# Kernel optimization log

Hardware: AMD Instinct MI355X
Metric: run time of the kernel (lower is better)

Reference implementation:

```python
import jax, jax.numpy as jnp
import numpy as np

D = 160          # volume side
WIN = 32         # spatial window size (box filter, matches fftconvolve with ones kernel)
NUM_MIN = 100    # minimum count constraint (constraint.min_number_from_ratio)
K_CCL = 16       # fixed number of 6-neighbor min-propagation sweeps (CCL definition)
NUM_BINS = 4096  # fixed histogram bins replacing data-dependent np.unique
VALUES = (0, 1, 2)
LIST_LABELS = (1,)
NUM_LABELS = 2
HALF = WIN // 2


def _box1d(x, w, ax):
    # 'same' box-sum along one axis via cumsum (== fftconvolve with ones(w))
    left = w // 2
    right = w - 1 - left
    x = jnp.moveaxis(x, ax, -1)
    pads = [(0, 0)] * (x.ndim - 1) + [(left, right)]
    c = jnp.cumsum(jnp.pad(x, pads), axis=-1)
    c = jnp.pad(c, [(0, 0)] * (x.ndim - 1) + [(1, 0)])
    out = c[..., w:] - c[..., :-w]
    return jnp.moveaxis(out, -1, ax)


def box_sum(x, w):
    for ax in range(x.ndim):
        x = _box1d(x, w, ax)
    return x


def _shift(a, s, ax, fill):
    # shift by s along ax, filling vacated border with `fill`
    r = jnp.roll(a, s, axis=ax)
    n = a.shape[ax]
    co = jnp.arange(n).reshape([n if i == ax else 1 for i in range(a.ndim)])
    bad = (co < s) if s > 0 else (co >= n + s)
    return jnp.where(bad, fill, r)


def label_size_map(seg):
    # create_label_size_map: connected-component labeling (6-connectivity,
    # K_CCL min-propagation sweeps) then replace each component by its size.
    n_vox = seg.size
    big = jnp.int32(n_vox + 2)
    idx = (jnp.arange(n_vox, dtype=jnp.int32) + 1).reshape(seg.shape)
    lab0 = jnp.where(seg, idx, big)

    def step(_, lab):
        m = lab
        for ax in range(seg.ndim):
            for s in (1, -1):
                m = jnp.minimum(m, _shift(lab, s, ax, big))
        return jnp.where(seg, m, big)

    lab = jax.lax.fori_loop(0, K_CCL, step, lab0)
    labels = jnp.where(seg, lab, 0)  # background -> label 0
    cnt = jnp.zeros(n_vox + 1, jnp.float32).at[labels.ravel()].add(1.0)
    return jnp.where(seg, cnt[labels], 0.0)


def _proba_weights(candidates, mean_list):
    # create_probability_weights: reciprocal-histogram weighting over rounded
    # mean component sizes (fixed NUM_BINS integer bins; bin 0 = non-candidate).
    pw = jnp.ones_like(candidates)
    for m in mean_list:
        possible = candidates * m
        idx = jnp.clip(jnp.round(possible), 0, NUM_BINS - 1).astype(jnp.int32)
        hist = jnp.zeros(NUM_BINS, jnp.float32).at[idx.ravel()].add(1.0)
        numb = jnp.sum(hist[1:])
        rec = jnp.where(hist[1:] > 0, numb / jnp.maximum(hist[1:], 1.0), 0.0)
        ph = rec / jnp.sum(rec)
        ph_full = jnp.concatenate([jnp.zeros(1, jnp.float32), ph])
        pw = pw * ph_full[idx]
    return pw / jnp.sum(pw)


def setup_inputs() -> dict:
    key = jax.random.key(0)
    data = jax.random.randint(key, (D, D, D), 0, 3).astype(jnp.float32)
    return {"data": data}


def reference(data):
    data = jnp.round(data)
    inner = tuple(s - 2 * HALF for s in data.shape)
    final = jnp.pad(jnp.ones(inner, jnp.float32), [(HALF, HALF)] * 3)
    mean_list = []
    valid_others = []
    for v in VALUES:
        seg = data == v
        segf = seg.astype(jnp.float32)
        lsize = label_size_map(seg)
        cw = box_sum(segf, WIN)                              # counts_window
        valid = (cw > max(NUM_MIN, 1)).astype(jnp.float32)   # valid_places
        cs = box_sum(lsize * valid, WIN)                     # counts_size
        mean = jnp.where(cw > 0, cs / jnp.maximum(cw, 1.0), 0.0)
        if v in LIST_LABELS:
            mean_list.append(mean)
            final = final * valid
        else:
            valid_others.append(valid)
    for vo in valid_others:
        final = final + vo
    num_labels_add = max(NUM_LABELS - len(LIST_LABELS), 0)
    candidates = (final >= num_labels_add + 1).astype(jnp.float32)
    proba_fin = _proba_weights(candidates, mean_list)
    return candidates, proba_fin
```

## Files before the change

kernel.cpp:

```cpp
#include <hip/hip_runtime.h>
#include <cmath>

#define D 160
#define DD (D*D)
#define NVOX (D*D*D)
#define BIGV (NVOX + 2)
#define NBINS 4096
#define HALF 16
#define RGRID 800
#define SGRID 1000
#define ZGRID 1000

template<int MODE>
__device__ __forceinline__ void rot_block(
    const void* __restrict__ vin, unsigned* __restrict__ out, int bi, int tid)
{
    __shared__ unsigned tin[32][161];
    __shared__ unsigned filt[160][33];
    int L0 = bi * 32;
    size_t base = (size_t)L0 * D;

    if (MODE == 0) {
        const float4* s4 = (const float4*)((const float*)vin + base);
        for (int i = tid; i < 32 * (D / 4); i += 512) {
            float4 v = s4[i];
            int e = i * 4, r = e / D, c = e - r * D;
            float rr;
            rr = rintf(v.x); tin[r][c]   = (rr==0.f) | ((rr==1.f)?0x10000u:0u);
            rr = rintf(v.y); tin[r][c+1] = (rr==0.f) | ((rr==1.f)?0x10000u:0u);
            rr = rintf(v.z); tin[r][c+2] = (rr==0.f) | ((rr==1.f)?0x10000u:0u);
            rr = rintf(v.w); tin[r][c+3] = (rr==0.f) | ((rr==1.f)?0x10000u:0u);
        }
    } else {
        const uint4* s4 = (const uint4*)((const unsigned*)vin + base);
        for (int i = tid; i < 32 * (D / 4); i += 512) {
            uint4 v = s4[i];
            int e = i * 4, r = e / D, c = e - r * D;
            tin[r][c] = v.x; tin[r][c+1] = v.y; tin[r][c+2] = v.z; tin[r][c+3] = v.w;
        }
    }
    __syncthreads();

    {
        int r = tid & 31, s = tid >> 5;
        int i0 = 10 * s;
        const unsigned* ln = tin[r];
        unsigned sum = 0u;
        int jlo = i0 - 16; if (jlo < 0) jlo = 0;
        int jhi = i0 + 15; if (jhi > D - 1) jhi = D - 1;
        for (int j = jlo; j <= jhi; ++j) sum += ln[j];
        #pragma unroll
        for (int k = 0; k < 10; ++k) {
            int i = i0 + k;
            filt[i][r] = sum;
            int add = i + 16, rem = i - 16;
            if (add <= D - 1) sum += ln[add];
            if (rem >= 0)     sum -= ln[rem];
        }
    }
    __syncthreads();

    int r = tid & 31;
    for (int c = (tid >> 5); c < D; c += 16)
        out[(size_t)c * DD + L0 + r] = filt[c][r];
}

__global__ __launch_bounds__(256) void box_rot_f32_g_kernel(
    const int* __restrict__ lab, const int* __restrict__ cnt,
    const unsigned* __restrict__ cwp, float* __restrict__ out)
{
    __shared__ float tin[32][161];
    __shared__ float filt[160][33];
    int L0 = blockIdx.x * 32;
    size_t base = (size_t)L0 * D;

    const int4*  lab4 = (const int4*)(lab + base);
    const uint4* cw4  = (const uint4*)(cwp + base);
    for (int i = threadIdx.x; i < 32 * (D / 4); i += 256) {
        int4 l = lab4[i];
        uint4 cw = cw4[i];
        int e = i * 4, r = e / D, c = e - r * D;
        tin[r][c]   = (l.x != BIGV && (cw.x >> 16) > 100u) ? (float)cnt[l.x] : 0.f;
        tin[r][c+1] = (l.y != BIGV && (cw.y >> 16) > 100u) ? (float)cnt[l.y] : 0.f;
        tin[r][c+2] = (l.z != BIGV && (cw.z >> 16) > 100u) ? (float)cnt[l.z] : 0.f;
        tin[r][c+3] = (l.w != BIGV && (cw.w >> 16) > 100u) ? (float)cnt[l.w] : 0.f;
    }
    __syncthreads();

    {
        int r = threadIdx.x & 31, s = threadIdx.x >> 5;
        int i0 = 20 * s;
        const float* ln = tin[r];
        float sum = 0.f;
        int jlo = i0 - 16; if (jlo < 0) jlo = 0;
        int jhi = i0 + 15; if (jhi > D - 1) jhi = D - 1;
        for (int j = jlo; j <= jhi; ++j) sum += ln[j];
        #pragma unroll 4
        for (int k = 0; k < 20; ++k) {
            int i = i0 + k;
            filt[i][r] = sum;
            int add = i + 16, rem = i - 16;
            if (add <= D - 1) sum += ln[add];
            if (rem >= 0)     sum -= ln[rem];
        }
    }
    __syncthreads();

    int r = threadIdx.x & 31;
    for (int c = (threadIdx.x >> 5); c < D; c += 8)
        out[(size_t)c * DD + L0 + r] = filt[c][r];
}

__global__ __launch_bounds__(256) void box_rot_f32_kernel(
    const float* __restrict__ fin, float* __restrict__ out)
{
    __shared__ float tin[32][161];
    __shared__ float filt[160][33];
    int L0 = blockIdx.x * 32;
    size_t base = (size_t)L0 * D;

    const float4* s4 = (const float4*)(fin + base);
    for (int i = threadIdx.x; i < 32 * (D / 4); i += 256) {
        float4 v = s4[i];
        int e = i * 4, r = e / D, c = e - r * D;
        tin[r][c] = v.x; tin[r][c+1] = v.y; tin[r][c+2] = v.z; tin[r][c+3] = v.w;
    }
    __syncthreads();

    {
        int r = threadIdx.x & 31, s = threadIdx.x >> 5;
        int i0 = 20 * s;
        const float* ln = tin[r];
        float sum = 0.f;
        int jlo = i0 - 16; if (jlo < 0) jlo = 0;
        int jhi = i0 + 15; if (jhi > D - 1) jhi = D - 1;
        for (int j = jlo; j <= jhi; ++j) sum += ln[j];
        #pragma unroll 4
        for (int k = 0; k < 20; ++k) {
            int i = i0 + k;
            filt[i][r] = sum;
            int add = i + 16, rem = i - 16;
            if (add <= D - 1) sum += ln[add];
            if (rem >= 0)     sum -= ln[rem];
        }
    }
    __syncthreads();

    int r = threadIdx.x & 31;
    for (int c = (threadIdx.x >> 5); c < D; c += 8)
        out[(size_t)c * DD + L0 + r] = filt[c][r];
}

__global__ __launch_bounds__(256) void box_rot_fin_kernel(
    const float* __restrict__ fin, const unsigned* __restrict__ cwp,
    float* __restrict__ cand, unsigned short* __restrict__ idxbuf,
    int* __restrict__ partial)
{
    __shared__ float tin[32][161];
    __shared__ float filt[160][33];
    __shared__ int lh[NBINS];
    for (int i = threadIdx.x; i < NBINS; i += 256) lh[i] = 0;

    int L0 = blockIdx.x * 32;
    size_t base = (size_t)L0 * D;
    const float4* s4 = (const float4*)(fin + base);
    for (int i = threadIdx.x; i < 32 * (D / 4); i += 256) {
        float4 v = s4[i];
        int e = i * 4, r = e / D, c = e - r * D;
        tin[r][c] = v.x; tin[r][c+1] = v.y; tin[r][c+2] = v.z; tin[r][c+3] = v.w;
    }
    __syncthreads();

    {
        int r = threadIdx.x & 31, s = threadIdx.x >> 5;
        int i0 = 20 * s;
        const float* ln = tin[r];
        float sum = 0.f;
        int jlo = i0 - 16; if (jlo < 0) jlo = 0;
        int jhi = i0 + 15; if (jhi > D - 1) jhi = D - 1;
        for (int j = jlo; j <= jhi; ++j) sum += ln[j];
        #pragma unroll 4
        for (int k = 0; k < 20; ++k) {
            int i = i0 + k;
            filt[i][r] = sum;
            int add = i + 16, rem = i - 16;
            if (add <= D - 1) sum += ln[add];
            if (rem >= 0)     sum -= ln[rem];
        }
    }
    __syncthreads();

    int r = threadIdx.x & 31;
    int L = L0 + r;
    int y = L / D, z = L - (L / D) * D;
    bool byz = (y >= HALF && y < D - HALF && z >= HALF && z < D - HALF);
    int wy = min(y + 15, D - 1) - max(y - 16, 0) + 1;
    int wz = min(z + 15, D - 1) - max(z - 16, 0) + 1;
    for (int c = (threadIdx.x >> 5); c < D; c += 8) {
        int p = c * DD + L;
        unsigned pk = cwp[p];
        unsigned cw0 = pk & 0xFFFFu;
        unsigned cw1 = pk >> 16;
        int wx = min(c + 15, D - 1) - max(c - 16, 0) + 1;
        unsigned cw2 = (unsigned)(wx * wy * wz) - cw0 - cw1;
        float v0 = (cw0 > 100u) ? 1.f : 0.f;
        float v1 = (cw1 > 100u) ? 1.f : 0.f;
        float v2 = (cw2 > 100u) ? 1.f : 0.f;
        float border = (byz && c >= HALF && c < D - HALF) ? 1.f : 0.f;
        float cd = (border * v1 + v0 + v2 >= 2.f) ? 1.f : 0.f;
        cand[p] = cd;
        float mean = (cw1 > 0u) ? filt[c][r] / fmaxf((float)cw1, 1.f) : 0.f;
        int idx = (int)rintf(cd * mean);
        idx = min(max(idx, 0), NBINS - 1);
        idxbuf[p] = (unsigned short)idx;
        if (idx != 0) atomicAdd(&lh[idx], 1);
    }
    __syncthreads();
    int* po = partial + blockIdx.x * NBINS;
    for (int i = threadIdx.x; i < NBINS; i += 256) po[i] = lh[i];
}

__device__ __forceinline__ int min6(int c, int a, int b, int d, int e, int f, int g) {
    if (c == BIGV) return BIGV;
    return min(min(min(c, a), min(b, d)), min(min(e, f), g));
}

__device__ __forceinline__ int4 min7_run(int4 c, int lm, int rm,
                                         int4 ym, int4 yp, int4 xm, int4 xp) {
    int4 o;
    o.x = min6(c.x, lm,  c.y, ym.x, yp.x, xm.x, xp.x);
    o.y = min6(c.y, c.x, c.z, ym.y, yp.y, xm.y, xp.y);
    o.z = min6(c.z, c.y, c.w, ym.z, yp.z, xm.z, xp.z);
    o.w = min6(c.w, c.z, rm,  ym.w, yp.w, xm.w, xp.w);
    return o;
}

__device__ __forceinline__ void wave_count(int l, int lane, int* __restrict__ cnt) {
    unsigned long long remaining = __ballot(l != BIGV);
    while (remaining) {
        int leader = __ffsll((unsigned long long)remaining) - 1;
        int ll = __shfl(l, leader, 64);
        unsigned long long mm = __ballot(l == ll);
        if (lane == leader) atomicAdd(&cnt[ll], (int)__popcll(mm & remaining));
        remaining &= ~mm;
    }
}

__device__ __forceinline__ int4 cls4(float4 v, int p0) {
    int4 l;
    l.x = (rintf(v.x) == 1.f) ? (p0 + 1) : BIGV;
    l.y = (rintf(v.y) == 1.f) ? (p0 + 2) : BIGV;
    l.z = (rintf(v.z) == 1.f) ? (p0 + 3) : BIGV;
    l.w = (rintf(v.w) == 1.f) ? (p0 + 4) : BIGV;
    return l;
}

struct LabLd {
    const int* __restrict__ a;
    __device__ __forceinline__ int4 v(int p) const { return ((const int4*)a)[p >> 2]; }
    __device__ __forceinline__ int  s(int p) const { return a[p]; }
};
struct DataLd {
    const float* __restrict__ a;
    __device__ __forceinline__ int4 v(int p) const { return cls4(((const float4*)a)[p >> 2], p); }
    __device__ __forceinline__ int  s(int p) const { return (rintf(a[p]) == 1.f) ? (p + 1) : BIGV; }
};

template<typename LDT, int COUNT>
__device__ __forceinline__ void sweep_block(
    LDT ld, int* __restrict__ outp, int* __restrict__ cnt, int b, int tid)
{
    const int4 BIG4 = make_int4(BIGV, BIGV, BIGV, BIGV);
    int sb = (b & 7) * (SGRID / 8) + (b >> 3);
    int lane = tid & 63;
    int wv   = tid >> 6;
    int wbase = sb * 4096 + wv * 512;
    int pA = wbase + 4 * lane;
    int pB = pA + 256;

    int4 cA = ld.v(pA), cB = ld.v(pB);

    int zA = pA % D, zB = pB % D;
    int lmA = __shfl_up(cA.w, 1);
    int rmA = __shfl_down(cA.x, 1);
    int lmB = __shfl_up(cB.w, 1);
    int rmB = __shfl_down(cB.x, 1);
    int stA = __shfl(cB.x, 0, 64);
    int stB = __shfl(cA.w, 63, 64);
    if (lane == 63) rmA = stA;
    if (lane == 0)  lmB = stB;
    if (zA == 0)          lmA = BIGV;
    else if (lane == 0)   lmA = ld.s(pA - 1);
    if (zA == D - 4)      rmA = BIGV;
    if (zB == 0)          lmB = BIGV;
    if (zB == D - 4)      rmB = BIGV;
    else if (lane == 63)  rmB = ld.s(pB + 4);

    int rA = pA / D, yA = rA % D, xA = rA / D;
    int4 ylA = (yA > 0)     ? ld.v(pA - D)  : BIG4;
    int4 yhA = (yA < D - 1) ? ld.v(pA + D)  : BIG4;
    int4 xlA = (xA > 0)     ? ld.v(pA - DD) : BIG4;
    int4 xhA = (xA < D - 1) ? ld.v(pA + DD) : BIG4;
    int4 oA = min7_run(cA, lmA, rmA, ylA, yhA, xlA, xhA);

    int rB = pB / D, yB = rB % D, xB = rB / D;
    int4 ylB = (yB > 0)     ? ld.v(pB - D)  : BIG4;
    int4 yhB = (yB < D - 1) ? ld.v(pB + D)  : BIG4;
    int4 xlB = (xB > 0)     ? ld.v(pB - DD) : BIG4;
    int4 xhB = (xB < D - 1) ? ld.v(pB + DD) : BIG4;
    int4 oB = min7_run(cB, lmB, rmB, ylB, yhB, xlB, xhB);

    int4* out4 = (int4*)outp;
    out4[pA >> 2] = oA; out4[pB >> 2] = oB;

    if (COUNT) {
        wave_count(oA.x, lane, cnt);
        wave_count(oA.y, lane, cnt);
        wave_count(oA.z, lane, cnt);
        wave_count(oA.w, lane, cnt);
        wave_count(oB.x, lane, cnt);
        wave_count(oB.y, lane, cnt);
        wave_count(oB.z, lane, cnt);
        wave_count(oB.w, lane, cnt);
    }
}

__global__ __launch_bounds__(512) void ccl_sweep_kernel(
    const int* __restrict__ lab, int* __restrict__ outp)
{
    LabLd ld{lab};
    sweep_block<LabLd, 0>(ld, outp, nullptr, blockIdx.x, threadIdx.x);
}

__global__ __launch_bounds__(512) void ccl_sweep_count_kernel(
    const int* __restrict__ lab, int* __restrict__ outp, int* __restrict__ cnt)
{
    LabLd ld{lab};
    sweep_block<LabLd, 1>(ld, outp, cnt, blockIdx.x, threadIdx.x);
}

template<int MODE>
__global__ __launch_bounds__(512) void sweep_rot_kernel(
    const float* __restrict__ data, const int* __restrict__ labsrc,
    int* __restrict__ swdst,
    const void* __restrict__ rin, unsigned* __restrict__ rout)
{
    if ((int)blockIdx.x < SGRID) {
        if (MODE == 0) {
            DataLd ld{data};
            sweep_block<DataLd, 0>(ld, swdst, nullptr, blockIdx.x, threadIdx.x);
        } else {
            LabLd ld{labsrc};
            sweep_block<LabLd, 0>(ld, swdst, nullptr, blockIdx.x, threadIdx.x);
        }
    } else {
        rot_block<MODE>(rin, rout, blockIdx.x - SGRID, threadIdx.x);
    }
}

__global__ __launch_bounds__(512) void sweep_zero_kernel(
    const int* __restrict__ labsrc, int* __restrict__ swdst,
    int* __restrict__ zbuf)
{
    if ((int)blockIdx.x < SGRID) {
        LabLd ld{labsrc};
        sweep_block<LabLd, 0>(ld, swdst, nullptr, blockIdx.x, threadIdx.x);
    } else {
        int zb = blockIdx.x - SGRID;
        int t = (zb * 512 + threadIdx.x) * 2;
        const int4 z4 = make_int4(0, 0, 0, 0);
        ((int4*)zbuf)[t] = z4; ((int4*)zbuf)[t + 1] = z4;
        if (zb == 0 && threadIdx.x == 0) zbuf[NVOX] = 0;
    }
}

__global__ __launch_bounds__(256) void hist_reduce_kernel(
    const int* __restrict__ partial, int* __restrict__ hist)
{
    int bin = blockIdx.x * 256 + threadIdx.x;
    int s = 0;
    #pragma unroll 4
    for (int b = 0; b < RGRID; ++b) s += partial[b * NBINS + bin];
    hist[bin] = s;
}

__global__ __launch_bounds__(256) void hist_post_kernel(
    const int* __restrict__ hist, float* __restrict__ ph_full,
    float* __restrict__ Sout)
{
    __shared__ float red[256];
    int t = threadIdx.x;

    float loc = 0.f;
    for (int b = t; b < NBINS; b += 256)
        if (b >= 1) loc += (float)hist[b];
    red[t] = loc; __syncthreads();
    for (int o = 128; o > 0; o >>= 1) { if (t < o) red[t] += red[t + o]; __syncthreads(); }
    float numb = red[0]; __syncthreads();

    loc = 0.f;
    for (int b = t; b < NBINS; b += 256) {
        float r = 0.f;
        if (b >= 1) {
            int h = hist[b];
            if (h > 0) r = numb / (float)h;
        }
        ph_full[b] = r;
        loc += r;
    }
    red[t] = loc; __syncthreads();
    for (int o = 128; o > 0; o >>= 1) { if (t < o) red[t] += red[t + o]; __syncthreads(); }
    float sumrec = red[0]; __syncthreads();
    float inv_sumrec = (sumrec > 0.f) ? 1.f / sumrec : 0.f;

    loc = 0.f;
    for (int b = t; b < NBINS; b += 256) {
        float ph = (b >= 1) ? ph_full[b] * inv_sumrec : 0.f;
        ph_full[b] = ph;
        loc += ph * (float)hist[b];
    }
    red[t] = loc; __syncthreads();
    for (int o = 128; o > 0; o >>= 1) { if (t < o) red[t] += red[t + o]; __syncthreads(); }
    if (t == 0) Sout[0] = (red[0] > 0.f) ? red[0] : 1.f;
}

__global__ __launch_bounds__(256) void proba_kernel(
    const unsigned short* __restrict__ idxbuf,
    const float* __restrict__ ph_full, const float* __restrict__ Sv,
    float* __restrict__ outp)
{
    int t = blockIdx.x * blockDim.x + threadIdx.x;
    ushort4 i4 = ((const ushort4*)idxbuf)[t];
    float inv = 1.f / Sv[0];
    float4 o;
    o.x = ph_full[i4.x] * inv;
    o.y = ph_full[i4.y] * inv;
    o.z = ph_full[i4.z] * inv;
    o.w = ph_full[i4.w] * inv;
    ((float4*)outp)[t] = o;
}

extern "C" void kernel_launch(void* const* d_in, const int* in_sizes, int n_in,
                              void* d_out, int out_size, void* d_ws, size_t ws_size,
                              hipStream_t stream)
{
    const float* data = (const float*)d_in[0];
    float* out   = (float*)d_out;
    float* cand  = out;
    float* proba = out + NVOX;

    char* ws = (char*)d_ws;
    const size_t NB = (size_t)NVOX * sizeof(float);
    float* W1 = (float*)(ws);
    float* W2 = (float*)(ws + NB);
    float* W3 = (float*)(ws + 2 * NB);
    int*   W4 = (int*)(ws + 3 * NB);
    int*   cnt  = W4;
    float* ph   = (float*)(ws + 4 * NB + 16);
    int*   hist = (int*)  (ws + 4 * NB + 16 + NBINS * 4);
    float* Sv   = (float*)(ws + 4 * NB + 16 + 2 * NBINS * 4);
    unsigned short* idxbuf = (unsigned short*)cnt;
    int* partial = (int*)W2;

    dim3 rb(256), rg(RGRID);
    dim3 sbk(512);
    dim3 sg(SGRID);
    dim3 srg(SGRID + RGRID);
    dim3 szg(SGRID + ZGRID);
    dim3 pb(256), pg(NVOX / 4 / 256);

    sweep_rot_kernel<0><<<srg, sbk, 0, stream>>>(data, nullptr, (int*)W2,
                                                 data, (unsigned*)W1);
    sweep_rot_kernel<1><<<srg, sbk, 0, stream>>>(nullptr, (int*)W2, W4,
                                                 W1, (unsigned*)W3);
    sweep_rot_kernel<1><<<srg, sbk, 0, stream>>>(nullptr, W4, (int*)W2,
                                                 W3, (unsigned*)W1);
    unsigned* cwp = (unsigned*)W1;

    sweep_zero_kernel<<<szg, sbk, 0, stream>>>((int*)W2, (int*)W3, W4);

    for (int i = 0; i < 11; ++i) {
        const int* src = (i & 1) ? (int*)W2 : (int*)W3;
        int*       dst = (i & 1) ? (int*)W3 : (int*)W2;
        ccl_sweep_kernel<<<sg, sbk, 0, stream>>>(src, dst);
    }
    ccl_sweep_count_kernel<<<sg, sbk, 0, stream>>>((int*)W2, (int*)W3, cnt);
    int* lab = (int*)W3;

    box_rot_f32_g_kernel<<<rg, rb, 0, stream>>>(lab, cnt, cwp, W2);
    box_rot_f32_kernel<<<rg, rb, 0, stream>>>(W2, W3);
    box_rot_fin_kernel<<<rg, rb, 0, stream>>>(W3, cwp, cand, idxbuf, partial);

    hist_reduce_kernel<<<dim3(16), dim3(256), 0, stream>>>(partial, hist);
    hist_post_kernel<<<1, 256, 0, stream>>>(hist, ph, Sv);
    proba_kernel<<<pg, pb, 0, stream>>>(idxbuf, ph, Sv, proba);
}
```

Baseline: 391.0 us.

## Compute candidates inside a CCL sweep launch and merge histogram kernels via ticket

Moves the candidate-mask computation out of the final box kernel into extra blocks appended to the first plain CCL sweep launch, so it overlaps with the sweep and the final kernel writes less. The histogram reduction and post-processing are merged into one launch, where the last block to finish (tracked by an atomic ticket counter) does the normalisation. This removes one kernel launch and shortens the serial tail. The cost is extra fences and atomics, plus a ticket that must be reset on every call.

```diff
diff --git a/kernel.cpp b/kernel.cpp
--- a/kernel.cpp
+++ b/kernel.cpp
@@ -10,6 +10,7 @@
 #define RGRID 800
 #define SGRID 1000
 #define ZGRID 1000
+#define CGRID 800
 
 template<int MODE>
 __device__ __forceinline__ void rot_block(
@@ -153,8 +154,7 @@
 
 __global__ __launch_bounds__(256) void box_rot_fin_kernel(
     const float* __restrict__ fin, const unsigned* __restrict__ cwp,
-    float* __restrict__ cand, unsigned short* __restrict__ idxbuf,
-    int* __restrict__ partial)
+    unsigned short* __restrict__ idxbuf, int* __restrict__ partial)
 {
     __shared__ float tin[32][161];
     __shared__ float filt[160][33];
@@ -208,7 +208,6 @@
         float v2 = (cw2 > 100u) ? 1.f : 0.f;
         float border = (byz && c >= HALF && c < D - HALF) ? 1.f : 0.f;
         float cd = (border * v1 + v0 + v2 >= 2.f) ? 1.f : 0.f;
-        cand[p] = cd;
         float mean = (cw1 > 0u) ? filt[c][r] / fmaxf((float)cw1, 1.f) : 0.f;
         int idx = (int)rintf(cd * mean);
         idx = min(max(idx, 0), NBINS - 1);
@@ -360,7 +359,7 @@
 
 __global__ __launch_bounds__(512) void sweep_zero_kernel(
     const int* __restrict__ labsrc, int* __restrict__ swdst,
-    int* __restrict__ zbuf)
+    int* __restrict__ zbuf, int* __restrict__ ticket)
 {
     if ((int)blockIdx.x < SGRID) {
         LabLd ld{labsrc};
@@ -370,42 +369,115 @@
         int t = (zb * 512 + threadIdx.x) * 2;
         const int4 z4 = make_int4(0, 0, 0, 0);
         ((int4*)zbuf)[t] = z4; ((int4*)zbuf)[t + 1] = z4;
-        if (zb == 0 && threadIdx.x == 0) zbuf[NVOX] = 0;
-    }
-}
-
-__global__ __launch_bounds__(256) void hist_reduce_kernel(
-    const int* __restrict__ partial, int* __restrict__ hist)
-{
-    int bin = blockIdx.x * 256 + threadIdx.x;
+        if (zb == 0 && threadIdx.x == 0) { zbuf[NVOX] = 0; ticket[0] = 0; }
+    }
+}
+
+__global__ __launch_bounds__(512) void sweep_cand_kernel(
+    const int* __restrict__ labsrc, int* __restrict__ swdst,
+    const unsigned* __restrict__ cwp, float* __restrict__ cand)
+{
+    if ((int)blockIdx.x < SGRID) {
+        LabLd ld{labsrc};
+        sweep_block<LabLd, 0>(ld, swdst, nullptr, blockIdx.x, threadIdx.x);
+        return;
+    }
+    int t0 = (blockIdx.x - SGRID) * 512 + threadIdx.x;
+    const uint4* cw4 = (const uint4*)cwp;
+    float4* c4 = (float4*)cand;
+    for (int q = t0; q < NVOX / 4; q += CGRID * 512) {
+        int p0 = q * 4;
+        int z0 = p0 % D;
+        int r  = p0 / D;
+        int y  = r % D;
+        int x  = r / D;
+        int wy = min(y + 15, D - 1) - max(y - 16, 0) + 1;
+        int wx = min(x + 15, D - 1) - max(x - 16, 0) + 1;
+        bool bxy = (y >= HALF && y < D - HALF && x >= HALF && x < D - HALF);
+        uint4 pk = cw4[q];
+        float4 o;
+        {
+            unsigned c0 = pk.x & 0xFFFFu, c1 = pk.x >> 16;
+            int z = z0, wz = min(z + 15, D - 1) - max(z - 16, 0) + 1;
+            unsigned c2 = (unsigned)(wx * wy * wz) - c0 - c1;
+            float v0 = (c0 > 100u) ? 1.f : 0.f, v1 = (c1 > 100u) ? 1.f : 0.f, v2 = (c2 > 100u) ? 1.f : 0.f;
+            float border = (bxy && z >= HALF && z < D - HALF) ? 1.f : 0.f;
+            o.x = (border * v1 + v0 + v2 >= 2.f) ? 1.f : 0.f;
+        }
+        {
+            unsigned c0 = pk.y & 0xFFFFu, c1 = pk.y >> 16;
+            int z = z0 + 1, wz = min(z + 15, D - 1) - max(z - 16, 0) + 1;
+            unsigned c2 = (unsigned)(wx * wy * wz) - c0 - c1;
+            float v0 = (c0 > 100u) ? 1.f : 0.f, v1 = (c1 > 100u) ? 1.f : 0.f, v2 = (c2 > 100u) ? 1.f : 0.f;
+            float border = (bxy && z >= HALF && z < D - HALF) ? 1.f : 0.f;
+            o.y = (border * v1 + v0 + v2 >= 2.f) ? 1.f : 0.f;
+        }
+        {
+            unsigned c0 = pk.z & 0xFFFFu, c1 = pk.z >> 16;
+            int z = z0 + 2, wz = min(z + 15, D - 1) - max(z - 16, 0) + 1;
+            unsigned c2 = (unsigned)(wx * wy * wz) - c0 - c1;
+            float v0 = (c0 > 100u) ? 1.f : 0.f, v1 = (c1 > 100u) ? 1.f : 0.f, v2 = (c2 > 100u) ? 1.f : 0.f;
+            float border = (bxy && z >= HALF && z < D - HALF) ? 1.f : 0.f;
+            o.z = (border * v1 + v0 + v2 >= 2.f) ? 1.f : 0.f;
+        }
+        {
+            unsigned c0 = pk.w & 0xFFFFu, c1 = pk.w >> 16;
+            int z = z0 + 3, wz = min(z + 15, D - 1) - max(z - 16, 0) + 1;
+            unsigned c2 = (unsigned)(wx * wy * wz) - c0 - c1;
+            float v0 = (c0 > 100u) ? 1.f : 0.f, v1 = (c1 > 100u) ? 1.f : 0.f, v2 = (c2 > 100u) ? 1.f : 0.f;
+            float border = (bxy && z >= HALF && z < D - HALF) ? 1.f : 0.f;
+            o.w = (border * v1 + v0 + v2 >= 2.f) ? 1.f : 0.f;
+        }
+        c4[q] = o;
+    }
+}
+
+__global__ __launch_bounds__(256) void hist_rp_kernel(
+    const int* __restrict__ partial, int* __restrict__ hist,
+    float* __restrict__ ph_full, float* __restrict__ Sout,
+    int* __restrict__ ticket)
+{
+    int t = threadIdx.x;
+    int bin = blockIdx.x * 256 + t;
     int s = 0;
     #pragma unroll 4
     for (int b = 0; b < RGRID; ++b) s += partial[b * NBINS + bin];
-    hist[bin] = s;
-}
-
-__global__ __launch_bounds__(256) void hist_post_kernel(
-    const int* __restrict__ hist, float* __restrict__ ph_full,
-    float* __restrict__ Sout)
-{
+    __hip_atomic_store(&hist[bin], s, __ATOMIC_RELAXED, __HIP_MEMORY_SCOPE_AGENT);
+    __threadfence();
+    __syncthreads();
+    __shared__ int lastblk;
+    if (t == 0) lastblk = (atomicAdd(ticket, 1) == gridDim.x - 1) ? 1 : 0;
+    __syncthreads();
+    if (!lastblk) return;
+
     __shared__ float red[256];
-    int t = threadIdx.x;
+    int hv[16];
+    #pragma unroll
+    for (int k = 0; k < 16; ++k)
+        hv[k] = __hip_atomic_load(&hist[t + k * 256], __ATOMIC_RELAXED,
+                                  __HIP_MEMORY_SCOPE_AGENT);
 
     float loc = 0.f;
-    for (int b = t; b < NBINS; b += 256)
-        if (b >= 1) loc += (float)hist[b];
+    #pragma unroll
+    for (int k = 0; k < 16; ++k) {
+        int b = t + k * 256;
+        if (b >= 1) loc += (float)hv[k];
+    }
     red[t] = loc; __syncthreads();
     for (int o = 128; o > 0; o >>= 1) { if (t < o) red[t] += red[t + o]; __syncthreads(); }
     float numb = red[0]; __syncthreads();
 
+    float rv[16];
     loc = 0.f;
-    for (int b = t; b < NBINS; b += 256) {
+    #pragma unroll
+    for (int k = 0; k < 16; ++k) {
+        int b = t + k * 256;
         float r = 0.f;
         if (b >= 1) {
-            int h = hist[b];
+            int h = hv[k];
             if (h > 0) r = numb / (float)h;
         }
-        ph_full[b] = r;
+        rv[k] = r;
         loc += r;
     }
     red[t] = loc; __syncthreads();
@@ -414,10 +486,12 @@
     float inv_sumrec = (sumrec > 0.f) ? 1.f / sumrec : 0.f;
 
     loc = 0.f;
-    for (int b = t; b < NBINS; b += 256) {
-        float ph = (b >= 1) ? ph_full[b] * inv_sumrec : 0.f;
+    #pragma unroll
+    for (int k = 0; k < 16; ++k) {
+        int b = t + k * 256;
+        float ph = (b >= 1) ? rv[k] * inv_sumrec : 0.f;
         ph_full[b] = ph;
-        loc += ph * (float)hist[b];
+        loc += ph * (float)hv[k];
     }
     red[t] = loc; __syncthreads();
     for (int o = 128; o > 0; o >>= 1) { if (t < o) red[t] += red[t + o]; __syncthreads(); }
@@ -459,6 +533,7 @@
     float* ph   = (float*)(ws + 4 * NB + 16);
     int*   hist = (int*)  (ws + 4 * NB + 16 + NBINS * 4);
     float* Sv   = (float*)(ws + 4 * NB + 16 + 2 * NBINS * 4);
+    int*   ticket = (int*)(ws + 4 * NB + 16 + 2 * NBINS * 4 + 8);
     unsigned short* idxbuf = (unsigned short*)cnt;
     int* partial = (int*)W2;
 
@@ -467,6 +542,7 @@
     dim3 sg(SGRID);
     dim3 srg(SGRID + RGRID);
     dim3 szg(SGRID + ZGRID);
+    dim3 scg(SGRID + CGRID);
     dim3 pb(256), pg(NVOX / 4 / 256);
 
     sweep_rot_kernel<0><<<srg, sbk, 0, stream>>>(data, nullptr, (int*)W2,
@@ -477,11 +553,13 @@
                                                  W3, (unsigned*)W1);
     unsigned* cwp = (unsigned*)W1;
 
-    sweep_zero_kernel<<<szg, sbk, 0, stream>>>((int*)W2, (int*)W3, W4);
-
-    for (int i = 0; i < 11; ++i) {
-        const int* src = (i & 1) ? (int*)W2 : (int*)W3;
-        int*       dst = (i & 1) ? (int*)W3 : (int*)W2;
+    sweep_zero_kernel<<<szg, sbk, 0, stream>>>((int*)W2, (int*)W3, W4, ticket);
+
+    sweep_cand_kernel<<<scg, sbk, 0, stream>>>((int*)W3, (int*)W2, cwp, cand);
+
+    for (int i = 0; i < 10; ++i) {
+        const int* src = (i & 1) ? (int*)W3 : (int*)W2;
+        int*       dst = (i & 1) ? (int*)W2 : (int*)W3;
         ccl_sweep_kernel<<<sg, sbk, 0, stream>>>(src, dst);
     }
     ccl_sweep_count_kernel<<<sg, sbk, 0, stream>>>((int*)W2, (int*)W3, cnt);
@@ -489,9 +567,8 @@
 
     box_rot_f32_g_kernel<<<rg, rb, 0, stream>>>(lab, cnt, cwp, W2);
     box_rot_f32_kernel<<<rg, rb, 0, stream>>>(W2, W3);
-    box_rot_fin_kernel<<<rg, rb, 0, stream>>>(W3, cwp, cand, idxbuf, partial);
-
-    hist_reduce_kernel<<<dim3(16), dim3(256), 0, stream>>>(partial, hist);
-    hist_post_kernel<<<1, 256, 0, stream>>>(hist, ph, Sv);
+    box_rot_fin_kernel<<<rg, rb, 0, stream>>>(W3, cwp, idxbuf, partial);
+
+    hist_rp_kernel<<<dim3(16), dim3(256), 0, stream>>>(partial, hist, ph, Sv, ticket);
     proba_kernel<<<pg, pb, 0, stream>>>(idxbuf, ph, Sv, proba);
 }
```

New measurement: 386.8 us. Within noise of the previous version (-1.1%).
